# Performance work log

Measured on AMD Instinct MI355X. Metric: run time of the kernel, lower is better.

## Reference

```python
import jax, jax.numpy as jnp
import numpy as np

N = 1_000_000
D = 128
NUM_CLASSES = 1000


def setup_inputs() -> dict:
    key = jax.random.key(0)
    k1, k2 = jax.random.split(key)
    embeddings = jax.random.normal(k1, (N, D), dtype=jnp.float32)
    labels = jax.random.randint(k2, (N,), 0, NUM_CLASSES, dtype=jnp.int64)
    return {"embeddings": embeddings, "labels": labels}


def reference(embeddings, labels):
    # Per-class mean via one-pass segment sums (equivalent to the torch
    # per-unique-label masked-mean loop, since all classes are present).
    sums = jax.ops.segment_sum(embeddings, labels, num_segments=NUM_CLASSES)  # [C, D]
    counts = jax.ops.segment_sum(
        jnp.ones((embeddings.shape[0],), dtype=embeddings.dtype), labels,
        num_segments=NUM_CLASSES)  # [C]
    class_means = sums / counts[:, None]  # [C, D]
    # torch.var default is unbiased (ddof=1)
    variance = jnp.var(class_means, axis=0, ddof=1).mean()
    return -variance
```

## Files before the change

### kernel.cpp

```cpp
#include <hip/hip_runtime.h>
#include <stdint.h>

#define NROWS 1000000
#define DDIM  128
#define NCLS  1000
#define SUMROWS 1024

#define GBLOCKS 512
#define NWAVES  (GBLOCKS * 8)
#define WCHUNK  256
#define TOTPAD  (NWAVES * WCHUNK)

typedef float f4 __attribute__((ext_vector_type(4)));

#define WS_SUMS    0
#define WS_COUNTS  131072
#define WS_CURSOR  132096
#define WS_VARD    133120
#define WS_ENTRIES 133376

__global__ __launch_bounds__(256) void zero_kernel(float* __restrict__ sums,
                                                   int* __restrict__ counts) {
    int t = blockIdx.x * 256 + threadIdx.x;
    f4 z = {0.0f, 0.0f, 0.0f, 0.0f};
    ((f4*)sums)[t] = z;
    if (t < SUMROWS) counts[t] = 0;
}

__global__ __launch_bounds__(256) void hist_kernel(const int* __restrict__ labels,
                                                   int* __restrict__ counts) {
    __shared__ int h[NCLS];
    for (int e = threadIdx.x; e < NCLS; e += 256) h[e] = 0;
    __syncthreads();
    for (int r = blockIdx.x * 256 + threadIdx.x; r < NROWS; r += 256 * 256)
        atomicAdd(&h[labels[r]], 1);
    __syncthreads();
    for (int e = threadIdx.x; e < NCLS; e += 256) atomicAdd(&counts[e], h[e]);
}

__global__ __launch_bounds__(1024) void scan_kernel(const int* __restrict__ counts,
                                                    int* __restrict__ cursor,
                                                    unsigned* __restrict__ entries) {
    if (threadIdx.x == 0) {
        int run = 0;
        for (int c = 0; c < NCLS; ++c) { cursor[c] = run; run += counts[c]; }
    }
    for (int i = NROWS + threadIdx.x; i < TOTPAD; i += 1024)
        entries[i] = (1023u << 20);
}

__global__ __launch_bounds__(256) void scatter_kernel(const int* __restrict__ labels,
                                                      int* __restrict__ cursor,
                                                      unsigned* __restrict__ entries) {
    for (int r = blockIdx.x * 256 + threadIdx.x; r < NROWS; r += 1024 * 256) {
        int lbl = labels[r];
        int pos = atomicAdd(&cursor[lbl], 1);
        entries[pos] = (unsigned)r | ((unsigned)lbl << 20);
    }
}

__global__ __launch_bounds__(512, 2) void gather_kernel(const float* __restrict__ emb,
                                                        const unsigned* __restrict__ entries,
                                                        float* __restrict__ sums) {
    const f4* emb4 = (const f4*)emb;
    const int wid  = blockIdx.x * 8 + (threadIdx.x >> 6);
    const int lane = threadIdx.x & 63;
    const int h    = lane >> 5;
    const int q    = lane & 31;
    const int wbase = wid * WCHUNK;

    f4 acc = {0.0f, 0.0f, 0.0f, 0.0f};
    unsigned cur = 0xFFFFFFFFu;

    for (int b = 0; b < WCHUNK / 64; ++b) {
        unsigned pk = entries[wbase + b * 64 + lane];
        #pragma unroll
        for (int g = 0; g < 4; ++g) {
            unsigned pks[8];
            f4 vv[8];
            #pragma unroll
            for (int u = 0; u < 8; ++u) {
                pks[u] = __shfl((int)pk, g * 16 + 2 * u + h);
                vv[u]  = __builtin_nontemporal_load(
                             &emb4[(size_t)(pks[u] & 0xFFFFFu) * 32 + q]);
            }
            #pragma unroll
            for (int u = 0; u < 8; ++u) {
                unsigned c = pks[u] >> 20;
                if (c != cur) {
                    if (cur < NCLS) {
                        unsafeAtomicAdd(&sums[cur * DDIM + q * 4 + 0], acc.x);
                        unsafeAtomicAdd(&sums[cur * DDIM + q * 4 + 1], acc.y);
                        unsafeAtomicAdd(&sums[cur * DDIM + q * 4 + 2], acc.z);
                        unsafeAtomicAdd(&sums[cur * DDIM + q * 4 + 3], acc.w);
                    }
                    f4 z = {0.0f, 0.0f, 0.0f, 0.0f};
                    acc = z;
                    cur = c;
                }
                acc += vv[u];
            }
        }
    }
    if (cur < NCLS) {
        unsafeAtomicAdd(&sums[cur * DDIM + q * 4 + 0], acc.x);
        unsafeAtomicAdd(&sums[cur * DDIM + q * 4 + 1], acc.y);
        unsafeAtomicAdd(&sums[cur * DDIM + q * 4 + 2], acc.z);
        unsafeAtomicAdd(&sums[cur * DDIM + q * 4 + 3], acc.w);
    }
}

__global__ __launch_bounds__(256) void var_kernel(const float* __restrict__ sums,
                                                  const int* __restrict__ counts,
                                                  float* __restrict__ var_d) {
    const int d = blockIdx.x;
    float s1 = 0.0f, s2 = 0.0f;
    for (int c = threadIdx.x; c < NCLS; c += 256) {
        float mv = sums[c * DDIM + d] / (float)counts[c];
        s1 += mv;
        s2 += mv * mv;
    }
    #pragma unroll
    for (int off = 32; off; off >>= 1) {
        s1 += __shfl_down(s1, off);
        s2 += __shfl_down(s2, off);
    }
    __shared__ float p1[4], p2[4];
    int wave = threadIdx.x >> 6, lane = threadIdx.x & 63;
    if (lane == 0) { p1[wave] = s1; p2[wave] = s2; }
    __syncthreads();
    if (threadIdx.x == 0) {
        float t1 = p1[0] + p1[1] + p1[2] + p1[3];
        float t2 = p2[0] + p2[1] + p2[2] + p2[3];
        var_d[d] = (t2 - t1 * t1 / (float)NCLS) / (float)(NCLS - 1);
    }
}

__global__ __launch_bounds__(64) void final_kernel(const float* __restrict__ var_d,
                                                   float* __restrict__ out) {
    float s = var_d[threadIdx.x] + var_d[threadIdx.x + 64];
    #pragma unroll
    for (int off = 32; off; off >>= 1) s += __shfl_down(s, off);
    if (threadIdx.x == 0) out[0] = -s / (float)DDIM;
}

extern "C" void kernel_launch(void* const* d_in, const int* in_sizes, int n_in,
                              void* d_out, int out_size, void* d_ws, size_t ws_size,
                              hipStream_t stream) {
    const float* emb    = (const float*)d_in[0];
    const int*   labels = (const int*)d_in[1];
    float*    wsf     = (float*)d_ws;
    int*      wsi     = (int*)d_ws;
    float*    sums    = wsf + WS_SUMS;
    int*      counts  = wsi + WS_COUNTS;
    int*      cursor  = wsi + WS_CURSOR;
    float*    var_d   = wsf + WS_VARD;
    unsigned* entries = (unsigned*)d_ws + WS_ENTRIES;
    float*    out     = (float*)d_out;

    hipLaunchKernelGGL(zero_kernel, dim3(128), dim3(256), 0, stream, sums, counts);
    hipLaunchKernelGGL(hist_kernel, dim3(256), dim3(256), 0, stream, labels, counts);
    hipLaunchKernelGGL(scan_kernel, dim3(1), dim3(1024), 0, stream, counts, cursor, entries);
    hipLaunchKernelGGL(scatter_kernel, dim3(1024), dim3(256), 0, stream, labels, cursor, entries);
    hipLaunchKernelGGL(gather_kernel, dim3(GBLOCKS), dim3(512), 0, stream, emb, entries, sums);
    hipLaunchKernelGGL(var_kernel, dim3(DDIM), dim3(256), 0, stream, sums, counts, var_d);
    hipLaunchKernelGGL(final_kernel, dim3(1), dim3(64), 0, stream, var_d, out);
}
```

Baseline: 861.4 us.

## Bucket gather entries by row segment and class, add dynamic chunk scheduling

```diff
diff --git a/kernel.cpp b/kernel.cpp
--- a/kernel.cpp
+++ b/kernel.cpp
@@ -4,48 +4,80 @@
 #define NROWS 1000000
 #define DDIM  128
 #define NCLS  1000
-#define SUMROWS 1024
-
+
+#define NSEG  32
+#define SEGSZ 31250
+#define NBUCK (NSEG * NCLS)
+
+#define CHUNK   128
+#define TOTPAD  1048576
+#define NCHUNK  (TOTPAD / CHUNK)
 #define GBLOCKS 512
-#define NWAVES  (GBLOCKS * 8)
-#define WCHUNK  256
-#define TOTPAD  (NWAVES * WCHUNK)
 
 typedef float f4 __attribute__((ext_vector_type(4)));
 
 #define WS_SUMS    0
-#define WS_COUNTS  131072
-#define WS_CURSOR  132096
-#define WS_VARD    133120
-#define WS_ENTRIES 133376
+#define WS_HIST    131072
+#define WS_CURSOR  163072
+#define WS_COUNTS  195072
+#define WS_VARD    196096
+#define WS_CTR     196224
+#define WS_ENTRIES 196608
 
 __global__ __launch_bounds__(256) void zero_kernel(float* __restrict__ sums,
-                                                   int* __restrict__ counts) {
+                                                   int* __restrict__ hist,
+                                                   int* __restrict__ ctr) {
     int t = blockIdx.x * 256 + threadIdx.x;
     f4 z = {0.0f, 0.0f, 0.0f, 0.0f};
     ((f4*)sums)[t] = z;
-    if (t < SUMROWS) counts[t] = 0;
+    if (t < NBUCK) hist[t] = 0;
+    if (t == 0) *ctr = 0;
 }
 
 __global__ __launch_bounds__(256) void hist_kernel(const int* __restrict__ labels,
-                                                   int* __restrict__ counts) {
+                                                   int* __restrict__ hist) {
     __shared__ int h[NCLS];
+    const int sid = blockIdx.x >> 3;
+    const int sl  = blockIdx.x & 7;
+    const int sb  = sid * SEGSZ;
+    const int lo  = sb + (SEGSZ * sl) / 8;
+    const int hi  = sb + (SEGSZ * (sl + 1)) / 8;
     for (int e = threadIdx.x; e < NCLS; e += 256) h[e] = 0;
     __syncthreads();
-    for (int r = blockIdx.x * 256 + threadIdx.x; r < NROWS; r += 256 * 256)
+    for (int r = lo + threadIdx.x; r < hi; r += 256)
         atomicAdd(&h[labels[r]], 1);
     __syncthreads();
-    for (int e = threadIdx.x; e < NCLS; e += 256) atomicAdd(&counts[e], h[e]);
-}
-
-__global__ __launch_bounds__(1024) void scan_kernel(const int* __restrict__ counts,
+    for (int e = threadIdx.x; e < NCLS; e += 256)
+        if (h[e]) atomicAdd(&hist[sid * NCLS + e], h[e]);
+}
+
+__global__ __launch_bounds__(1024) void scan_kernel(const int* __restrict__ hist,
                                                     int* __restrict__ cursor,
+                                                    int* __restrict__ counts,
                                                     unsigned* __restrict__ entries) {
-    if (threadIdx.x == 0) {
-        int run = 0;
-        for (int c = 0; c < NCLS; ++c) { cursor[c] = run; run += counts[c]; }
-    }
-    for (int i = NROWS + threadIdx.x; i < TOTPAD; i += 1024)
+    __shared__ int part[1024];
+    const int t  = threadIdx.x;
+    const int lo = (NBUCK * t) >> 10;
+    const int hi = (NBUCK * (t + 1)) >> 10;
+    int s = 0;
+    for (int i = lo; i < hi; ++i) s += hist[i];
+    part[t] = s;
+    __syncthreads();
+    for (int off = 1; off < 1024; off <<= 1) {
+        int v = 0;
+        if (t >= off) v = part[t - off];
+        __syncthreads();
+        if (t >= off) part[t] += v;
+        __syncthreads();
+    }
+    int run = part[t] - s;
+    for (int i = lo; i < hi; ++i) { cursor[i] = run; run += hist[i]; }
+    for (int c = t; c < NCLS; c += 1024) {
+        int cc = 0;
+        for (int sg = 0; sg < NSEG; ++sg) cc += hist[sg * NCLS + c];
+        counts[c] = cc;
+    }
+    for (int i = NROWS + t; i < TOTPAD; i += 1024)
         entries[i] = (1023u << 20);
 }
 
@@ -54,51 +86,58 @@
                                                       unsigned* __restrict__ entries) {
     for (int r = blockIdx.x * 256 + threadIdx.x; r < NROWS; r += 1024 * 256) {
         int lbl = labels[r];
-        int pos = atomicAdd(&cursor[lbl], 1);
+        int bkt = (r / SEGSZ) * NCLS + lbl;
+        int pos = atomicAdd(&cursor[bkt], 1);
         entries[pos] = (unsigned)r | ((unsigned)lbl << 20);
     }
 }
 
-__global__ __launch_bounds__(512, 2) void gather_kernel(const float* __restrict__ emb,
+__global__ __launch_bounds__(512, 4) void gather_kernel(const float* __restrict__ emb,
                                                         const unsigned* __restrict__ entries,
+                                                        int* __restrict__ ctr,
                                                         float* __restrict__ sums) {
     const f4* emb4 = (const f4*)emb;
-    const int wid  = blockIdx.x * 8 + (threadIdx.x >> 6);
     const int lane = threadIdx.x & 63;
     const int h    = lane >> 5;
     const int q    = lane & 31;
-    const int wbase = wid * WCHUNK;
 
     f4 acc = {0.0f, 0.0f, 0.0f, 0.0f};
     unsigned cur = 0xFFFFFFFFu;
 
-    for (int b = 0; b < WCHUNK / 64; ++b) {
-        unsigned pk = entries[wbase + b * 64 + lane];
-        #pragma unroll
-        for (int g = 0; g < 4; ++g) {
-            unsigned pks[8];
-            f4 vv[8];
+    for (;;) {
+        int ch = 0;
+        if (lane == 0) ch = atomicAdd(ctr, 1);
+        ch = __shfl(ch, 0);
+        if (ch >= NCHUNK) break;
+        const int cb = ch * CHUNK;
+        for (int b = 0; b < CHUNK / 64; ++b) {
+            unsigned pk = entries[cb + b * 64 + lane];
             #pragma unroll
-            for (int u = 0; u < 8; ++u) {
-                pks[u] = __shfl((int)pk, g * 16 + 2 * u + h);
-                vv[u]  = __builtin_nontemporal_load(
-                             &emb4[(size_t)(pks[u] & 0xFFFFFu) * 32 + q]);
-            }
-            #pragma unroll
-            for (int u = 0; u < 8; ++u) {
-                unsigned c = pks[u] >> 20;
-                if (c != cur) {
-                    if (cur < NCLS) {
-                        unsafeAtomicAdd(&sums[cur * DDIM + q * 4 + 0], acc.x);
-                        unsafeAtomicAdd(&sums[cur * DDIM + q * 4 + 1], acc.y);
-                        unsafeAtomicAdd(&sums[cur * DDIM + q * 4 + 2], acc.z);
-                        unsafeAtomicAdd(&sums[cur * DDIM + q * 4 + 3], acc.w);
+            for (int g = 0; g < 4; ++g) {
+                unsigned pks[8];
+                f4 vv[8];
+                #pragma unroll
+                for (int u = 0; u < 8; ++u) {
+                    pks[u] = __shfl((int)pk, g * 16 + 2 * u + h);
+                    vv[u]  = __builtin_nontemporal_load(
+                                 &emb4[(size_t)(pks[u] & 0xFFFFFu) * 32 + q]);
+                }
+                #pragma unroll
+                for (int u = 0; u < 8; ++u) {
+                    unsigned c = pks[u] >> 20;
+                    if (c != cur) {
+                        if (cur < NCLS) {
+                            unsafeAtomicAdd(&sums[cur * DDIM + q * 4 + 0], acc.x);
+                            unsafeAtomicAdd(&sums[cur * DDIM + q * 4 + 1], acc.y);
+                            unsafeAtomicAdd(&sums[cur * DDIM + q * 4 + 2], acc.z);
+                            unsafeAtomicAdd(&sums[cur * DDIM + q * 4 + 3], acc.w);
+                        }
+                        f4 z = {0.0f, 0.0f, 0.0f, 0.0f};
+                        acc = z;
+                        cur = c;
                     }
-                    f4 z = {0.0f, 0.0f, 0.0f, 0.0f};
-                    acc = z;
-                    cur = c;
+                    acc += vv[u];
                 }
-                acc += vv[u];
             }
         }
     }
@@ -152,17 +191,19 @@
     float*    wsf     = (float*)d_ws;
     int*      wsi     = (int*)d_ws;
     float*    sums    = wsf + WS_SUMS;
+    int*      hist    = wsi + WS_HIST;
+    int*      cursor  = wsi + WS_CURSOR;
     int*      counts  = wsi + WS_COUNTS;
-    int*      cursor  = wsi + WS_CURSOR;
     float*    var_d   = wsf + WS_VARD;
+    int*      ctr     = wsi + WS_CTR;
     unsigned* entries = (unsigned*)d_ws + WS_ENTRIES;
     float*    out     = (float*)d_out;
 
-    hipLaunchKernelGGL(zero_kernel, dim3(128), dim3(256), 0, stream, sums, counts);
-    hipLaunchKernelGGL(hist_kernel, dim3(256), dim3(256), 0, stream, labels, counts);
-    hipLaunchKernelGGL(scan_kernel, dim3(1), dim3(1024), 0, stream, counts, cursor, entries);
+    hipLaunchKernelGGL(zero_kernel, dim3(128), dim3(256), 0, stream, sums, hist, ctr);
+    hipLaunchKernelGGL(hist_kernel, dim3(256), dim3(256), 0, stream, labels, hist);
+    hipLaunchKernelGGL(scan_kernel, dim3(1), dim3(1024), 0, stream, hist, cursor, counts, entries);
     hipLaunchKernelGGL(scatter_kernel, dim3(1024), dim3(256), 0, stream, labels, cursor, entries);
-    hipLaunchKernelGGL(gather_kernel, dim3(GBLOCKS), dim3(512), 0, stream, emb, entries, sums);
+    hipLaunchKernelGGL(gather_kernel, dim3(GBLOCKS), dim3(512), 0, stream, emb, entries, ctr, sums);
     hipLaunchKernelGGL(var_kernel, dim3(DDIM), dim3(256), 0, stream, sums, counts, var_d);
     hipLaunchKernelGGL(final_kernel, dim3(1), dim3(64), 0, stream, var_d, out);
 }
```

After: 862.6 us. About the same (+0.1%).
